# Kernel optimization log

Hardware: AMD Instinct MI355X
Metric: run time of the kernel (lower is better)

## Reference

```python
import jax, jax.numpy as jnp
import numpy as np

N = 100000   # points
C = 256      # in_planes
K = 16       # nsample (idx holds 2*K neighbors)
L = 2        # num_mlplayer
NEG = 0.1    # LeakyReLU slope
EPS = 1e-5   # LayerNorm eps (torch default)

PARAM_KEYS = ['emb_w1','emb_g1','emb_b1','emb_w2','conv_w','pw_w1','pw_g1','pw_b1','pw_w2','pw_g2','pw_b2']


def layer_norm(x, g, b):
    m = x.mean(-1, keepdims=True)
    v = ((x - m) ** 2).mean(-1, keepdims=True)
    return (x - m) * jax.lax.rsqrt(v + EPS) * g + b


def calc_ppf(p, n, pg, ng):
    # standard 4-dim point-pair features: angle(n1,d), angle(n2,d), angle(n1,n2), ||d||
    d = pg - p[:, None, :]                                   # [N,2K,3]
    dist = jnp.linalg.norm(d, axis=-1, keepdims=True)
    def angle(a, b):
        cr = jnp.linalg.norm(jnp.cross(a, b), axis=-1, keepdims=True)
        dt = jnp.sum(a * b, axis=-1, keepdims=True)
        return jnp.arctan2(cr, dt)
    n1 = jnp.broadcast_to(n[:, None, :], pg.shape)
    return jnp.concatenate([angle(n1, d), angle(ng, d), angle(n1, ng), dist], -1)


def mlp_layer(p, x, idx, ppf, r, pr):
    # cart2sphere -> r-normalized radial distance, giving 4+1=5 embedding inputs
    d = p[idx] - p[:, None, :]                               # [N,K,3]
    sphere = jnp.linalg.norm(d, axis=-1, keepdims=True) / r  # [N,K,1]
    f5 = jnp.concatenate([ppf, sphere], -1)                  # [N,K,5]
    h = f5 @ pr['emb_w1']
    h = jax.nn.leaky_relu(layer_norm(h, pr['emb_g1'], pr['emb_b1']), NEG)
    pos = h @ pr['emb_w2']                                   # [N,K,C]
    g = x[idx] + pos                                         # gather + add
    # Partial_conv3 (split_cat): 1x1 conv (no bias) on first C//4 channels
    c4 = pr['conv_w'].shape[0]
    g1 = jnp.einsum('nkc,dc->nkd', g[..., :c4], pr['conv_w'])
    g = jnp.concatenate([g1, g[..., c4:]], -1)
    pooled = g.max(axis=1)                                   # max-pool over neighbors [N,C]
    h = pooled @ pr['pw_w1']
    h = jax.nn.leaky_relu(layer_norm(h, pr['pw_g1'], pr['pw_b1']), NEG)
    h = layer_norm(h @ pr['pw_w2'], pr['pw_g2'], pr['pw_b2'])
    return jax.nn.relu(h + x)                                # residual + relu


def setup_inputs():
    key = jax.random.key(0)
    ks = jax.random.split(key, 16)
    s = 0.02
    n = jax.random.normal(ks[2], (N, 3), jnp.float32)
    n = n / jnp.linalg.norm(n, axis=-1, keepdims=True)
    return {
        'p': jax.random.normal(ks[0], (N, 3), jnp.float32),
        'x': jax.random.normal(ks[1], (N, C), jnp.float32),
        'n': n,
        'idx': jax.random.randint(ks[3], (N, 2 * K), 0, N, jnp.int32),
        'r': jnp.ones((1,), jnp.float32),
        'emb_w1': jax.random.normal(ks[4], (L, 5, C), jnp.float32) * s,
        'emb_g1': jnp.ones((L, C), jnp.float32),
        'emb_b1': jnp.zeros((L, C), jnp.float32),
        'emb_w2': jax.random.normal(ks[5], (L, C, C), jnp.float32) * s,
        'conv_w': jax.random.normal(ks[6], (L, C // 4, C // 4), jnp.float32) * s,
        'pw_w1': jax.random.normal(ks[7], (L, C, 4 * C), jnp.float32) * s,
        'pw_g1': jnp.ones((L, 4 * C), jnp.float32),
        'pw_b1': jnp.zeros((L, 4 * C), jnp.float32),
        'pw_w2': jax.random.normal(ks[8], (L, 4 * C, C), jnp.float32) * s,
        'pw_g2': jnp.ones((L, C), jnp.float32),
        'pw_b2': jnp.zeros((L, C), jnp.float32),
        'proj_w': jax.random.normal(ks[9], (C, C), jnp.float32) * s,
        'proj_b': jnp.zeros((C,), jnp.float32),
    }


def reference(p, x, n, idx, r, emb_w1, emb_g1, emb_b1, emb_w2, conv_w,
              pw_w1, pw_g1, pw_b1, pw_w2, pw_g2, pw_b2, proj_w, proj_b):
    # idx is given -> group_idx = idx (queryandgroup branch skipped, as in source)
    ppf = calc_ppf(p, n, p[idx], n[idx])                     # [N,2K,4]
    idx_m, ppf_m = idx[:, :K], ppf[:, :K]                    # mlp branch uses first nsample
    stacked = [emb_w1, emb_g1, emb_b1, emb_w2, conv_w, pw_w1, pw_g1, pw_b1, pw_w2, pw_g2, pw_b2]
    h = x
    for l in range(L):
        pr = dict(zip(PARAM_KEYS, [a[l] for a in stacked]))
        h = mlp_layer(p, h, idx_m, ppf_m, r[0], pr)
    # proj_mlp; blocks=1 -> trans_block is an empty Sequential (identity)
    return h @ proj_w + proj_b
```

## Files before the change

### kernel.cpp

```cpp
#include <hip/hip_runtime.h>
#include <stdint.h>

#define N_PTS 100000
#define NPAD  100032

typedef unsigned short u16;
typedef unsigned int   u32;
using bf16x8 = __attribute__((ext_vector_type(8))) short;
using f32x4  = __attribute__((ext_vector_type(4))) float;

__device__ __forceinline__ u16 f2bf(float f) {
    u32 u = __float_as_uint(f);
    u += 0x7FFFu + ((u >> 16) & 1u);
    return (u16)(u >> 16);
}
__device__ __forceinline__ float bf2f(u16 h) {
    return __uint_as_float(((u32)h) << 16);
}

__global__ __launch_bounds__(256) void k_transpose_pad(
    const float* __restrict__ src, u16* __restrict__ dst,
    int Lc, int R, int Cc, int stride) {
    int t = blockIdx.x * 256 + threadIdx.x;
    int total = Lc * Cc * stride;
    if (t >= total) return;
    int l = t / (Cc * stride);
    int rem = t - l * (Cc * stride);
    int co = rem / stride;
    int ci = rem - co * stride;
    dst[t] = (ci < R) ? f2bf(src[((size_t)l * R + ci) * Cc + co]) : (u16)0;
}

__global__ __launch_bounds__(256) void k_cast_bf16(
    const float* __restrict__ src, u16* __restrict__ dst, int total) {
    int t = blockIdx.x * 256 + threadIdx.x;
    if (t < total) dst[t] = f2bf(src[t]);
}

__global__ __launch_bounds__(256) void k_castx8(
    const float* __restrict__ src, u16* __restrict__ dst, int total8) {
    int t = blockIdx.x * 256 + threadIdx.x;
    if (t >= total8) return;
    float4 a = *(const float4*)(src + (size_t)t * 8);
    float4 b = *(const float4*)(src + (size_t)t * 8 + 4);
    uint4 o;
    o.x = (u32)f2bf(a.x) | ((u32)f2bf(a.y) << 16);
    o.y = (u32)f2bf(a.z) | ((u32)f2bf(a.w) << 16);
    o.z = (u32)f2bf(b.x) | ((u32)f2bf(b.y) << 16);
    o.w = (u32)f2bf(b.z) | ((u32)f2bf(b.w) << 16);
    *(uint4*)(dst + (size_t)t * 8) = o;
}

__device__ __forceinline__ float angf(float ax, float ay, float az,
                                      float bx, float by, float bz) {
    float cx = ay * bz - az * by;
    float cy = az * bx - ax * bz;
    float cz = ax * by - ay * bx;
    float cr = sqrtf(cx * cx + cy * cy + cz * cz);
    float dt = ax * bx + ay * by + az * bz;
    return atan2f(cr, dt);
}

__global__ __launch_bounds__(256) void k_ppf(
    const float* __restrict__ p, const float* __restrict__ nrm,
    const int* __restrict__ idx, const float* __restrict__ r,
    u16* __restrict__ f5b) {
    int t = blockIdx.x * 256 + threadIdx.x;
    if (t >= N_PTS * 16) return;
    int i = t >> 4;
    int j = idx[(size_t)i * 32 + (t & 15)];
    float pix = p[(size_t)i*3], piy = p[(size_t)i*3+1], piz = p[(size_t)i*3+2];
    float pjx = p[(size_t)j*3], pjy = p[(size_t)j*3+1], pjz = p[(size_t)j*3+2];
    float dx = pjx - pix, dy = pjy - piy, dz = pjz - piz;
    float dist = sqrtf(dx*dx + dy*dy + dz*dz);
    float nix = nrm[(size_t)i*3], niy = nrm[(size_t)i*3+1], niz = nrm[(size_t)i*3+2];
    float njx = nrm[(size_t)j*3], njy = nrm[(size_t)j*3+1], njz = nrm[(size_t)j*3+2];
    float a1 = angf(nix, niy, niz, dx, dy, dz);
    float a2 = angf(njx, njy, njz, dx, dy, dz);
    float a3 = angf(nix, niy, niz, njx, njy, njz);
    float rinv = 1.0f / r[0];
    u16* o = f5b + (size_t)t * 5;
    o[0] = f2bf(a1); o[1] = f2bf(a2); o[2] = f2bf(a3);
    o[3] = f2bf(dist); o[4] = f2bf(dist * rinv);
}

__device__ __forceinline__ bf16x8 fixup_frag(const uint2* pk, int kt,
                                             int srcA, int srcB, bool hiT) {
    int aLx = __shfl((int)pk[2*kt].x,   srcA);
    int aHx = __shfl((int)pk[2*kt+1].x, srcA);
    int aLy = __shfl((int)pk[2*kt].y,   srcA);
    int aHy = __shfl((int)pk[2*kt+1].y, srcA);
    int bLx = __shfl((int)pk[2*kt].x,   srcB);
    int bHx = __shfl((int)pk[2*kt+1].x, srcB);
    int bLy = __shfl((int)pk[2*kt].y,   srcB);
    int bHy = __shfl((int)pk[2*kt+1].y, srcB);
    uint4 u;
    u.x = (u32)(hiT ? aHx : aLx);
    u.y = (u32)(hiT ? aHy : aLy);
    u.z = (u32)(hiT ? bHx : bLx);
    u.w = (u32)(hiT ? bHy : bLy);
    return *(bf16x8*)&u;
}

__global__ __launch_bounds__(512, 4) void k_neighbor(
    const u16*   __restrict__ xcur,
    const u16*   __restrict__ f5b,
    const int*   __restrict__ idx,
    const u16*   __restrict__ w1pad,
    const float* __restrict__ g1, const float* __restrict__ b1,
    const u16*   __restrict__ ew2tp,
    const u16*   __restrict__ convbf,
    u16*         __restrict__ pooledb)
{
    __shared__ u16 Bs[64 * 264];
    __shared__ u16 posw[8][2][16][72];
    __shared__ u16 pbounce[8][2][256];
    __shared__ int idxs[16][16];

    const int tid = threadIdx.x, w = tid >> 6, lane = tid & 63;
    const int rr = lane & 15, q = lane >> 4;
    const int i0 = blockIdx.x * 16;

    for (int o = tid * 16; o < 33792; o += 8192)
        *(uint4*)((char*)Bs + o) = *(const uint4*)((const char*)ew2tp + o);
    if (tid < 256)
        idxs[tid >> 4][tid & 15] = idx[(size_t)(i0 + (tid >> 4)) * 32 + (tid & 15)];

    const int srcA = rr + ((q & 1) << 5);
    const int srcB = srcA + 16;
    const bool hiT = (q >> 1) != 0;

    bf16x8 hfrag[2][8];
    #pragma unroll
    for (int rt = 0; rt < 2; ++rt) {
        const int pt = i0 + 2 * w + rt;
        bf16x8 a1;
        #pragma unroll
        for (int e = 0; e < 8; ++e) a1[e] = 0;
        if (q == 0) {
            const u16* fp = f5b + (size_t)(pt * 16 + rr) * 5;
            a1[0] = (short)fp[0]; a1[1] = (short)fp[1];
            a1[2] = (short)fp[2]; a1[3] = (short)fp[3];
            a1[4] = (short)fp[4];
        }
        f32x4 hacc[16];
        __builtin_amdgcn_s_setprio(1);
        #pragma unroll
        for (int ct = 0; ct < 16; ++ct) {
            bf16x8 aW = *(const bf16x8*)&w1pad[(ct * 16 + rr) * 32 + q * 8];
            f32x4 z = {0.f, 0.f, 0.f, 0.f};
            hacc[ct] = __builtin_amdgcn_mfma_f32_16x16x32_bf16(aW, a1, z, 0, 0, 0);
        }
        __builtin_amdgcn_s_setprio(0);
        float s = 0.f, z2 = 0.f;
        #pragma unroll
        for (int ct = 0; ct < 16; ++ct) {
            #pragma unroll
            for (int j = 0; j < 4; ++j) { float v = hacc[ct][j]; s += v; z2 += v * v; }
        }
        s  += __shfl_xor(s, 16);  s  += __shfl_xor(s, 32);
        z2 += __shfl_xor(z2, 16); z2 += __shfl_xor(z2, 32);
        float mean = s * (1.f / 256.f);
        float var = fmaxf(z2 * (1.f / 256.f) - mean * mean, 0.f);
        float rstd = 1.0f / sqrtf(var + 1e-5f);

        uint2 pk[16];
        #pragma unroll
        for (int ct = 0; ct < 16; ++ct) {
            const int c0 = ct * 16 + 4 * q;
            float4 gg = *(const float4*)&g1[c0];
            float4 bb = *(const float4*)&b1[c0];
            float v0 = (hacc[ct][0] - mean) * rstd * gg.x + bb.x;
            float v1 = (hacc[ct][1] - mean) * rstd * gg.y + bb.y;
            float v2 = (hacc[ct][2] - mean) * rstd * gg.z + bb.z;
            float v3 = (hacc[ct][3] - mean) * rstd * gg.w + bb.w;
            v0 = v0 > 0.f ? v0 : 0.1f * v0;
            v1 = v1 > 0.f ? v1 : 0.1f * v1;
            v2 = v2 > 0.f ? v2 : 0.1f * v2;
            v3 = v3 > 0.f ? v3 : 0.1f * v3;
            pk[ct].x = (u32)f2bf(v0) | ((u32)f2bf(v1) << 16);
            pk[ct].y = (u32)f2bf(v2) | ((u32)f2bf(v3) << 16);
        }
        #pragma unroll
        for (int kt = 0; kt < 8; ++kt)
            hfrag[rt][kt] = fixup_frag(pk, kt, srcA, srcB, hiT);
    }
    __syncthreads();

    const int ppt = lane >> 5, cl = lane & 31;
    const int* ixp = idxs[2 * w + ppt];

    #pragma unroll 1
    for (int p = 0; p < 4; ++p) {
        __builtin_amdgcn_s_setprio(1);
        #pragma unroll
        for (int nt4 = 0; nt4 < 4; ++nt4) {
            f32x4 a0 = {0.f,0.f,0.f,0.f}, a1v = {0.f,0.f,0.f,0.f};
            #pragma unroll
            for (int kb = 0; kb < 8; ++kb) {
                bf16x8 bb = *(const bf16x8*)&Bs[(nt4 * 16 + rr) * 264 + kb * 32 + q * 8];
                a0  = __builtin_amdgcn_mfma_f32_16x16x32_bf16(hfrag[0][kb], bb, a0, 0, 0, 0);
                a1v = __builtin_amdgcn_mfma_f32_16x16x32_bf16(hfrag[1][kb], bb, a1v, 0, 0, 0);
            }
            #pragma unroll
            for (int j = 0; j < 4; ++j) {
                posw[w][0][4 * q + j][nt4 * 16 + rr] = f2bf(a0[j]);
                posw[w][1][4 * q + j][nt4 * 16 + rr] = f2bf(a1v[j]);
            }
        }
        __builtin_amdgcn_s_setprio(0);
        if (p < 3) {
            __syncthreads();
            const char* src = (const char*)(ew2tp + (size_t)(p + 1) * 64 * 264);
            for (int o = tid * 16; o < 33792; o += 8192)
                *(uint4*)((char*)Bs + o) = *(const uint4*)(src + o);
        }
        if (p == 0) {
            #pragma unroll
            for (int pt = 0; pt < 2; ++pt) {
                const u16* xr = xcur + (size_t)idxs[2 * w + pt][rr] * 256;
                bf16x8 gA[2];
                #pragma unroll
                for (int kb = 0; kb < 2; ++kb) {
                    bf16x8 xa = *(const bf16x8*)(xr + kb * 32 + q * 8);
                    bf16x8 pv = *(const bf16x8*)&posw[w][pt][rr][kb * 32 + q * 8];
                    bf16x8 g;
                    #pragma unroll
                    for (int e = 0; e < 8; ++e)
                        g[e] = (short)f2bf(bf2f((u16)xa[e]) + bf2f((u16)pv[e]));
                    gA[kb] = g;
                }
                __builtin_amdgcn_s_setprio(1);
                #pragma unroll
                for (int cn = 0; cn < 4; ++cn) {
                    bf16x8 cB0 = *(const bf16x8*)&convbf[(cn * 16 + rr) * 64 + q * 8];
                    bf16x8 cB1 = *(const bf16x8*)&convbf[(cn * 16 + rr) * 64 + 32 + q * 8];
                    f32x4 z = {0.f,0.f,0.f,0.f};
                    f32x4 acc = __builtin_amdgcn_mfma_f32_16x16x32_bf16(gA[0], cB0, z, 0, 0, 0);
                    acc = __builtin_amdgcn_mfma_f32_16x16x32_bf16(gA[1], cB1, acc, 0, 0, 0);
                    float m = fmaxf(fmaxf(acc[0], acc[1]), fmaxf(acc[2], acc[3]));
                    m = fmaxf(m, __shfl_xor(m, 16));
                    m = fmaxf(m, __shfl_xor(m, 32));
                    if (lane < 16) pbounce[w][pt][cn * 16 + lane] = f2bf(m);
                }
                __builtin_amdgcn_s_setprio(0);
            }
        } else {
            const int cq = p * 64 + cl * 2;
            u32 xv[16];
            #pragma unroll
            for (int k = 0; k < 16; ++k)
                xv[k] = *(const u32*)(xcur + (size_t)ixp[k] * 256 + cq);
            float m0 = -3e38f, m1 = -3e38f;
            #pragma unroll
            for (int k = 0; k < 16; ++k) {
                u32 pv = *(const u32*)&posw[w][ppt][k][cl * 2];
                float gv0 = bf2f((u16)(pv & 0xffffu)) + bf2f((u16)(xv[k] & 0xffffu));
                float gv1 = bf2f((u16)(pv >> 16))     + bf2f((u16)(xv[k] >> 16));
                m0 = fmaxf(m0, gv0);
                m1 = fmaxf(m1, gv1);
            }
            *(u32*)&pbounce[w][ppt][cq] = (u32)f2bf(m0) | ((u32)f2bf(m1) << 16);
        }
        if (p < 3) __syncthreads();
    }
    {
        const int pt = lane >> 5, off = (lane & 31) * 8;
        uint4 v = *(const uint4*)&pbounce[w][pt][off];
        *(uint4*)(pooledb + (size_t)(i0 + 2 * w + pt) * 256 + off) = v;
    }
}

__global__ __launch_bounds__(512, 4) void k_pointwise(
    const u16* poolb,
    const u16* __restrict__ xresb,
    u16*       outb,
    const u16* __restrict__ b1t,
    const float* __restrict__ g1, const float* __restrict__ b1,
    const u16* __restrict__ b2t,
    const float* __restrict__ g2, const float* __restrict__ b2,
    int guardRes)
{
    __shared__ u16 hm[32 * 1032];
    __shared__ float pst[32][8][2];

    const int tid = threadIdx.x, w = tid >> 6, lane = tid & 63;
    const int rr = lane & 15, q = lane >> 4;
    const size_t R0 = (size_t)blockIdx.x * 32;

    bf16x8 afr[2][8];
    #pragma unroll
    for (int rt = 0; rt < 2; ++rt) {
        int ar = (int)R0 + rt * 16 + rr; if (ar >= N_PTS) ar = N_PTS - 1;
        const u16* arow = poolb + (size_t)ar * 256;
        #pragma unroll
        for (int kb = 0; kb < 8; ++kb)
            afr[rt][kb] = *(const bf16x8*)(arow + kb * 32 + q * 8);
    }

    #pragma unroll 2
    for (int ct = 0; ct < 8; ++ct) {
        const int co = w * 128 + ct * 16 + rr;
        const u16* bp = b1t + (size_t)co * 256 + q * 8;
        bf16x8 bb[8];
        #pragma unroll
        for (int kb = 0; kb < 8; ++kb) bb[kb] = *(const bf16x8*)(bp + kb * 32);
        f32x4 a0 = {0.f,0.f,0.f,0.f}, a1v = {0.f,0.f,0.f,0.f};
        __builtin_amdgcn_s_setprio(1);
        #pragma unroll
        for (int kb = 0; kb < 8; ++kb) {
            a0  = __builtin_amdgcn_mfma_f32_16x16x32_bf16(afr[0][kb], bb[kb], a0, 0, 0, 0);
            a1v = __builtin_amdgcn_mfma_f32_16x16x32_bf16(afr[1][kb], bb[kb], a1v, 0, 0, 0);
        }
        __builtin_amdgcn_s_setprio(0);
        #pragma unroll
        for (int j = 0; j < 4; ++j) {
            hm[(4 * q + j) * 1032 + co]      = f2bf(a0[j]);
            hm[(16 + 4 * q + j) * 1032 + co] = f2bf(a1v[j]);
        }
    }
    __syncthreads();

    {
        const int row = tid >> 4;
        const int t16 = tid & 15;
        u32* hm32 = (u32*)hm;
        const int base = row * 516;
        float s = 0.f, z = 0.f;
        #pragma unroll 8
        for (int e = 0; e < 32; ++e) {
            u32 pk = hm32[base + t16 + 16 * e];
            float v0 = bf2f((u16)(pk & 0xffffu)), v1 = bf2f((u16)(pk >> 16));
            s += v0 + v1; z += v0 * v0 + v1 * v1;
        }
        s += __shfl_xor(s, 1); s += __shfl_xor(s, 2);
        s += __shfl_xor(s, 4); s += __shfl_xor(s, 8);
        z += __shfl_xor(z, 1); z += __shfl_xor(z, 2);
        z += __shfl_xor(z, 4); z += __shfl_xor(z, 8);
        float mean = s * (1.f / 1024.f);
        float var = fmaxf(z * (1.f / 1024.f) - mean * mean, 0.f);
        float rstd = 1.0f / sqrtf(var + 1e-5f);
        #pragma unroll 4
        for (int e = 0; e < 32; ++e) {
            const int cidx = t16 + 16 * e;
            u32 pk = hm32[base + cidx];
            const int c = cidx * 2;
            float2 gg = *(const float2*)&g1[c];
            float2 bbv = *(const float2*)&b1[c];
            float v0 = (bf2f((u16)(pk & 0xffffu)) - mean) * rstd * gg.x + bbv.x;
            float v1 = (bf2f((u16)(pk >> 16))     - mean) * rstd * gg.y + bbv.y;
            v0 = v0 > 0.f ? v0 : 0.1f * v0;
            v1 = v1 > 0.f ? v1 : 0.1f * v1;
            hm32[base + cidx] = (u32)f2bf(v0) | ((u32)f2bf(v1) << 16);
        }
    }
    __syncthreads();

    f32x4 acc2[2][2];
    #pragma unroll
    for (int ct = 0; ct < 2; ++ct) {
        const int cB = w * 32 + ct * 16 + rr;
        const u16* bp = b2t + (size_t)cB * 1024 + q * 8;
        f32x4 c0 = {0.f,0.f,0.f,0.f}, c1 = {0.f,0.f,0.f,0.f};
        __builtin_amdgcn_s_setprio(1);
        #pragma unroll 8
        for (int kb = 0; kb < 32; ++kb) {
            bf16x8 b  = *(const bf16x8*)(bp + kb * 32);
            bf16x8 a0 = *(const bf16x8*)&hm[rr * 1032 + kb * 32 + q * 8];
            bf16x8 a1 = *(const bf16x8*)&hm[(16 + rr) * 1032 + kb * 32 + q * 8];
            c0 = __builtin_amdgcn_mfma_f32_16x16x32_bf16(a0, b, c0, 0, 0, 0);
            c1 = __builtin_amdgcn_mfma_f32_16x16x32_bf16(a1, b, c1, 0, 0, 0);
        }
        __builtin_amdgcn_s_setprio(0);
        acc2[0][ct] = c0; acc2[1][ct] = c1;
    }

    #pragma unroll
    for (int rt = 0; rt < 2; ++rt) {
        #pragma unroll
        for (int j = 0; j < 4; ++j) {
            float s = acc2[rt][0][j] + acc2[rt][1][j];
            float z = acc2[rt][0][j] * acc2[rt][0][j] + acc2[rt][1][j] * acc2[rt][1][j];
            s += __shfl_xor(s, 1); s += __shfl_xor(s, 2);
            s += __shfl_xor(s, 4); s += __shfl_xor(s, 8);
            z += __shfl_xor(z, 1); z += __shfl_xor(z, 2);
            z += __shfl_xor(z, 4); z += __shfl_xor(z, 8);
            if (rr == 0) {
                pst[rt * 16 + 4 * q + j][w][0] = s;
                pst[rt * 16 + 4 * q + j][w][1] = z;
            }
        }
    }
    __syncthreads();

    #pragma unroll
    for (int rt = 0; rt < 2; ++rt) {
        float mean2[4], rstd2[4];
        #pragma unroll
        for (int j = 0; j < 4; ++j) {
            const int row = rt * 16 + 4 * q + j;
            float s = 0.f, z = 0.f;
            #pragma unroll
            for (int k = 0; k < 8; ++k) { s += pst[row][k][0]; z += pst[row][k][1]; }
            float mean = s * (1.f / 256.f);
            float var = fmaxf(z * (1.f / 256.f) - mean * mean, 0.f);
            mean2[j] = mean;
            rstd2[j] = 1.0f / sqrtf(var + 1e-5f);
        }
        #pragma unroll
        for (int ct = 0; ct < 2; ++ct) {
            const int c = w * 32 + ct * 16 + rr;
            const float gg = g2[c], bb = b2[c];
            #pragma unroll
            for (int j = 0; j < 4; ++j) {
                const size_t row = R0 + rt * 16 + 4 * q + j;
                float v = (acc2[rt][ct][j] - mean2[j]) * rstd2[j] * gg + bb;
                float xv = 0.f;
                if (!guardRes || row < (size_t)N_PTS) xv = bf2f(xresb[row * 256 + c]);
                float o = v + xv;
                outb[row * 256 + c] = f2bf(o > 0.f ? o : 0.f);
            }
        }
    }
}

__global__ __launch_bounds__(512, 4) void k_proj(
    const u16*   __restrict__ xinb,
    const u16*   __restrict__ pjtp,
    const float* __restrict__ pb,
    float*       __restrict__ out)
{
    __shared__ u16 Bs[128 * 264];
    const int tid = threadIdx.x, w = tid >> 6, lane = tid & 63;
    const int rr = lane & 15, q = lane >> 4;
    const size_t R0 = (size_t)blockIdx.x * 128 + (size_t)w * 16;

    int arn = (int)R0 + rr; if (arn >= N_PTS) arn = N_PTS - 1;
    const u16* arow = xinb + (size_t)arn * 256;
    bf16x8 afr[8];
    #pragma unroll
    for (int kb = 0; kb < 8; ++kb)
        afr[kb] = *(const bf16x8*)(arow + kb * 32 + q * 8);

    #pragma unroll 1
    for (int h = 0; h < 2; ++h) {
        if (h) __syncthreads();
        for (int o = tid * 16; o < 67584; o += 8192)
            *(uint4*)((char*)Bs + o) = *(const uint4*)((const char*)(pjtp + h * 128 * 264) + o);
        __syncthreads();
        #pragma unroll 2
        for (int nt8 = 0; nt8 < 8; ++nt8) {
            f32x4 acc = {0.f, 0.f, 0.f, 0.f};
            __builtin_amdgcn_s_setprio(1);
            #pragma unroll
            for (int kb = 0; kb < 8; ++kb) {
                bf16x8 b = *(const bf16x8*)&Bs[(nt8 * 16 + rr) * 264 + kb * 32 + q * 8];
                acc = __builtin_amdgcn_mfma_f32_16x16x32_bf16(afr[kb], b, acc, 0, 0, 0);
            }
            __builtin_amdgcn_s_setprio(0);
            const int c = h * 128 + nt8 * 16 + rr;
            const float bias = pb[c];
            #pragma unroll
            for (int j = 0; j < 4; ++j) {
                const size_t row = R0 + 4 * q + j;
                if (row < (size_t)N_PTS) out[row * 256 + c] = acc[j] + bias;
            }
        }
    }
}

extern "C" void kernel_launch(void* const* d_in, const int* in_sizes, int n_in,
                              void* d_out, int out_size, void* d_ws, size_t ws_size,
                              hipStream_t stream) {
    const float* p      = (const float*)d_in[0];
    const float* x      = (const float*)d_in[1];
    const float* nn     = (const float*)d_in[2];
    const int*   idx    = (const int*)d_in[3];
    const float* r      = (const float*)d_in[4];
    const float* emb_w1 = (const float*)d_in[5];
    const float* emb_g1 = (const float*)d_in[6];
    const float* emb_b1 = (const float*)d_in[7];
    const float* emb_w2 = (const float*)d_in[8];
    const float* conv_w = (const float*)d_in[9];
    const float* pw_w1  = (const float*)d_in[10];
    const float* pw_g1  = (const float*)d_in[11];
    const float* pw_b1  = (const float*)d_in[12];
    const float* pw_w2  = (const float*)d_in[13];
    const float* pw_g2  = (const float*)d_in[14];
    const float* pw_b2  = (const float*)d_in[15];
    const float* proj_w = (const float*)d_in[16];
    const float* proj_b = (const float*)d_in[17];
    float* out = (float*)d_out;

    char* ws = (char*)d_ws;
    const size_t SZB = (size_t)NPAD * 256 * sizeof(u16);
    u16* xb0 = (u16*)ws;
    u16* PB  = (u16*)(ws + SZB);
    u16* h1B = (u16*)(ws + 2 * SZB);
    u16* f5b = (u16*)(ws + 3 * SZB);
    u16* wb  = f5b + (size_t)N_PTS * 16 * 5;
    u16* ew2tp  = wb;
    u16* pjtp   = ew2tp + 2 * 256 * 264;
    u16* w1pad  = pjtp + 256 * 264;
    u16* convbf = w1pad + 2 * 256 * 32;
    u16* b1t    = convbf + 2 * 64 * 64;
    u16* b2t    = b1t + 2 * 1024 * 256;

    k_transpose_pad<<<(2*256*264 + 255)/256, 256, 0, stream>>>(emb_w2, ew2tp, 2, 256, 256, 264);
    k_transpose_pad<<<(256*264 + 255)/256, 256, 0, stream>>>(proj_w, pjtp, 1, 256, 256, 264);
    k_transpose_pad<<<(2*256*32 + 255)/256, 256, 0, stream>>>(emb_w1, w1pad, 2, 5, 256, 32);
    k_transpose_pad<<<(2*1024*256 + 255)/256, 256, 0, stream>>>(pw_w1, b1t, 2, 256, 1024, 256);
    k_transpose_pad<<<(2*256*1024 + 255)/256, 256, 0, stream>>>(pw_w2, b2t, 2, 1024, 256, 1024);
    k_cast_bf16<<<(2*64*64 + 255)/256, 256, 0, stream>>>(conv_w, convbf, 2*64*64);

    k_castx8<<<(N_PTS*256/8 + 255)/256, 256, 0, stream>>>(x, xb0, N_PTS*256/8);
    k_ppf<<<(N_PTS * 16 + 255)/256, 256, 0, stream>>>(p, nn, idx, r, f5b);

    k_neighbor<<<N_PTS/16, 512, 0, stream>>>(xb0, f5b, idx, w1pad, emb_g1, emb_b1,
                                             ew2tp, convbf, PB);
    k_pointwise<<<NPAD/32, 512, 0, stream>>>(PB, xb0, h1B, b1t, pw_g1, pw_b1,
                                             b2t, pw_g2, pw_b2, 1);
    k_neighbor<<<N_PTS/16, 512, 0, stream>>>(h1B, f5b, idx, w1pad + 256*32,
                                             emb_g1 + 256, emb_b1 + 256,
                                             ew2tp + 256*264, convbf + 64*64, xb0);
    k_pointwise<<<NPAD/32, 512, 0, stream>>>(xb0, h1B, PB, b1t + 1024*256,
                                             pw_g1 + 1024, pw_b1 + 1024,
                                             b2t + 256*1024, pw_g2 + 256, pw_b2 + 256, 0);
    k_proj<<<(NPAD + 127)/128, 512, 0, stream>>>(PB, pjtp, proj_b, out);
}
```

Baseline: 2.127 ms.

## Halve neighbor-kernel LDS staging to 32-column chunks and double occupancy hint

The neighbor kernel now stages the embedding weight in 32-column chunks instead of 64, which roughly halves its shared-memory buffers. It raises the launch-bounds minimum blocks per CU from 4 to 8. The 4-iteration loop is unrolled into an 8-stage explicit schedule in which gathered x loads for the pooling path are issued a stage ahead and consumed across two pooling stages. This aims for more resident blocks to hide gather latency, at the cost of twice as many barriers and weight-staging rounds and tighter register limits that could cause spills.

```diff
diff --git a/kernel.cpp b/kernel.cpp
--- a/kernel.cpp
+++ b/kernel.cpp
@@ -102,7 +102,7 @@
     return *(bf16x8*)&u;
 }
 
-__global__ __launch_bounds__(512, 4) void k_neighbor(
+__global__ __launch_bounds__(512, 8) void k_neighbor(
     const u16*   __restrict__ xcur,
     const u16*   __restrict__ f5b,
     const int*   __restrict__ idx,
@@ -112,8 +112,8 @@
     const u16*   __restrict__ convbf,
     u16*         __restrict__ pooledb)
 {
-    __shared__ u16 Bs[64 * 264];
-    __shared__ u16 posw[8][2][16][72];
+    __shared__ u16 Bs[32 * 264];
+    __shared__ u16 posw[8][2][16][40];
     __shared__ u16 pbounce[8][2][256];
     __shared__ int idxs[16][16];
 
@@ -121,7 +121,7 @@
     const int rr = lane & 15, q = lane >> 4;
     const int i0 = blockIdx.x * 16;
 
-    for (int o = tid * 16; o < 33792; o += 8192)
+    for (int o = tid * 16; o < 16896; o += 8192)
         *(uint4*)((char*)Bs + o) = *(const uint4*)((const char*)ew2tp + o);
     if (tid < 256)
         idxs[tid >> 4][tid & 15] = idx[(size_t)(i0 + (tid >> 4)) * 32 + (tid & 15)];
@@ -190,80 +190,139 @@
     const int ppt = lane >> 5, cl = lane & 31;
     const int* ixp = idxs[2 * w + ppt];
 
-    #pragma unroll 1
-    for (int p = 0; p < 4; ++p) {
+    auto do_gemm = [&]() {
         __builtin_amdgcn_s_setprio(1);
         #pragma unroll
-        for (int nt4 = 0; nt4 < 4; ++nt4) {
+        for (int nt2 = 0; nt2 < 2; ++nt2) {
             f32x4 a0 = {0.f,0.f,0.f,0.f}, a1v = {0.f,0.f,0.f,0.f};
             #pragma unroll
             for (int kb = 0; kb < 8; ++kb) {
-                bf16x8 bb = *(const bf16x8*)&Bs[(nt4 * 16 + rr) * 264 + kb * 32 + q * 8];
+                bf16x8 bb = *(const bf16x8*)&Bs[(nt2 * 16 + rr) * 264 + kb * 32 + q * 8];
                 a0  = __builtin_amdgcn_mfma_f32_16x16x32_bf16(hfrag[0][kb], bb, a0, 0, 0, 0);
                 a1v = __builtin_amdgcn_mfma_f32_16x16x32_bf16(hfrag[1][kb], bb, a1v, 0, 0, 0);
             }
             #pragma unroll
             for (int j = 0; j < 4; ++j) {
-                posw[w][0][4 * q + j][nt4 * 16 + rr] = f2bf(a0[j]);
-                posw[w][1][4 * q + j][nt4 * 16 + rr] = f2bf(a1v[j]);
+                posw[w][0][4 * q + j][nt2 * 16 + rr] = f2bf(a0[j]);
+                posw[w][1][4 * q + j][nt2 * 16 + rr] = f2bf(a1v[j]);
             }
         }
         __builtin_amdgcn_s_setprio(0);
-        if (p < 3) {
-            __syncthreads();
-            const char* src = (const char*)(ew2tp + (size_t)(p + 1) * 64 * 264);
-            for (int o = tid * 16; o < 33792; o += 8192)
-                *(uint4*)((char*)Bs + o) = *(const uint4*)(src + o);
-        }
-        if (p == 0) {
-            #pragma unroll
-            for (int pt = 0; pt < 2; ++pt) {
-                const u16* xr = xcur + (size_t)idxs[2 * w + pt][rr] * 256;
-                bf16x8 gA[2];
-                #pragma unroll
-                for (int kb = 0; kb < 2; ++kb) {
-                    bf16x8 xa = *(const bf16x8*)(xr + kb * 32 + q * 8);
-                    bf16x8 pv = *(const bf16x8*)&posw[w][pt][rr][kb * 32 + q * 8];
-                    bf16x8 g;
-                    #pragma unroll
-                    for (int e = 0; e < 8; ++e)
-                        g[e] = (short)f2bf(bf2f((u16)xa[e]) + bf2f((u16)pv[e]));
-                    gA[kb] = g;
-                }
-                __builtin_amdgcn_s_setprio(1);
-                #pragma unroll
-                for (int cn = 0; cn < 4; ++cn) {
-                    bf16x8 cB0 = *(const bf16x8*)&convbf[(cn * 16 + rr) * 64 + q * 8];
-                    bf16x8 cB1 = *(const bf16x8*)&convbf[(cn * 16 + rr) * 64 + 32 + q * 8];
-                    f32x4 z = {0.f,0.f,0.f,0.f};
-                    f32x4 acc = __builtin_amdgcn_mfma_f32_16x16x32_bf16(gA[0], cB0, z, 0, 0, 0);
-                    acc = __builtin_amdgcn_mfma_f32_16x16x32_bf16(gA[1], cB1, acc, 0, 0, 0);
-                    float m = fmaxf(fmaxf(acc[0], acc[1]), fmaxf(acc[2], acc[3]));
-                    m = fmaxf(m, __shfl_xor(m, 16));
-                    m = fmaxf(m, __shfl_xor(m, 32));
-                    if (lane < 16) pbounce[w][pt][cn * 16 + lane] = f2bf(m);
-                }
-                __builtin_amdgcn_s_setprio(0);
-            }
-        } else {
-            const int cq = p * 64 + cl * 2;
-            u32 xv[16];
-            #pragma unroll
-            for (int k = 0; k < 16; ++k)
-                xv[k] = *(const u32*)(xcur + (size_t)ixp[k] * 256 + cq);
+    };
+    auto stage_e = [&](int en) {
+        const char* src = (const char*)(ew2tp + (size_t)en * 32 * 264);
+        for (int o = tid * 16; o < 16896; o += 8192)
+            *(uint4*)((char*)Bs + o) = *(const uint4*)(src + o);
+    };
+    auto load_pair = [&](int pi, u32 (&xv)[16]) {
+        const int cq = pi * 64 + cl * 2;
+        #pragma unroll
+        for (int k = 0; k < 16; ++k)
+            xv[k] = *(const u32*)(xcur + (size_t)ixp[k] * 256 + cq);
+    };
+    auto pool_e = [&](int e, const u32 (&xv)[16]) {
+        if ((cl >> 4) == (e & 1)) {
+            const int t2 = (cl & 15) * 2;
             float m0 = -3e38f, m1 = -3e38f;
             #pragma unroll
             for (int k = 0; k < 16; ++k) {
-                u32 pv = *(const u32*)&posw[w][ppt][k][cl * 2];
-                float gv0 = bf2f((u16)(pv & 0xffffu)) + bf2f((u16)(xv[k] & 0xffffu));
-                float gv1 = bf2f((u16)(pv >> 16))     + bf2f((u16)(xv[k] >> 16));
-                m0 = fmaxf(m0, gv0);
-                m1 = fmaxf(m1, gv1);
-            }
-            *(u32*)&pbounce[w][ppt][cq] = (u32)f2bf(m0) | ((u32)f2bf(m1) << 16);
-        }
-        if (p < 3) __syncthreads();
-    }
+                u32 pv = *(const u32*)&posw[w][ppt][k][t2];
+                m0 = fmaxf(m0, bf2f((u16)(pv & 0xffffu)) + bf2f((u16)(xv[k] & 0xffffu)));
+                m1 = fmaxf(m1, bf2f((u16)(pv >> 16))     + bf2f((u16)(xv[k] >> 16)));
+            }
+            *(u32*)&pbounce[w][ppt][(e >> 1) * 64 + cl * 2] =
+                (u32)f2bf(m0) | ((u32)f2bf(m1) << 16);
+        }
+    };
+
+    bf16x8 gA0[2], gA1[2];
+    u32 xv[16];
+
+    do_gemm();
+    __syncthreads();
+    stage_e(1);
+    #pragma unroll
+    for (int pt = 0; pt < 2; ++pt) {
+        const u16* xr = xcur + (size_t)idxs[2 * w + pt][rr] * 256;
+        bf16x8 xa = *(const bf16x8*)(xr + q * 8);
+        bf16x8 pv = *(const bf16x8*)&posw[w][pt][rr][q * 8];
+        bf16x8 g;
+        #pragma unroll
+        for (int e = 0; e < 8; ++e)
+            g[e] = (short)f2bf(bf2f((u16)xa[e]) + bf2f((u16)pv[e]));
+        gA0[pt] = g;
+    }
+    __syncthreads();
+
+    do_gemm();
+    __syncthreads();
+    stage_e(2);
+    #pragma unroll
+    for (int pt = 0; pt < 2; ++pt) {
+        const u16* xr = xcur + (size_t)idxs[2 * w + pt][rr] * 256;
+        bf16x8 xa = *(const bf16x8*)(xr + 32 + q * 8);
+        bf16x8 pv = *(const bf16x8*)&posw[w][pt][rr][q * 8];
+        bf16x8 g;
+        #pragma unroll
+        for (int e = 0; e < 8; ++e)
+            g[e] = (short)f2bf(bf2f((u16)xa[e]) + bf2f((u16)pv[e]));
+        gA1[pt] = g;
+    }
+    #pragma unroll
+    for (int pt = 0; pt < 2; ++pt) {
+        __builtin_amdgcn_s_setprio(1);
+        #pragma unroll
+        for (int cn = 0; cn < 4; ++cn) {
+            bf16x8 cB0 = *(const bf16x8*)&convbf[(cn * 16 + rr) * 64 + q * 8];
+            bf16x8 cB1 = *(const bf16x8*)&convbf[(cn * 16 + rr) * 64 + 32 + q * 8];
+            f32x4 z = {0.f,0.f,0.f,0.f};
+            f32x4 acc = __builtin_amdgcn_mfma_f32_16x16x32_bf16(gA0[pt], cB0, z, 0, 0, 0);
+            acc = __builtin_amdgcn_mfma_f32_16x16x32_bf16(gA1[pt], cB1, acc, 0, 0, 0);
+            float m = fmaxf(fmaxf(acc[0], acc[1]), fmaxf(acc[2], acc[3]));
+            m = fmaxf(m, __shfl_xor(m, 16));
+            m = fmaxf(m, __shfl_xor(m, 32));
+            if (lane < 16) pbounce[w][pt][cn * 16 + lane] = f2bf(m);
+        }
+        __builtin_amdgcn_s_setprio(0);
+    }
+    load_pair(1, xv);
+    __syncthreads();
+
+    do_gemm();
+    __syncthreads();
+    stage_e(3);
+    pool_e(2, xv);
+    __syncthreads();
+
+    do_gemm();
+    __syncthreads();
+    stage_e(4);
+    pool_e(3, xv);
+    load_pair(2, xv);
+    __syncthreads();
+
+    do_gemm();
+    __syncthreads();
+    stage_e(5);
+    pool_e(4, xv);
+    __syncthreads();
+
+    do_gemm();
+    __syncthreads();
+    stage_e(6);
+    pool_e(5, xv);
+    load_pair(3, xv);
+    __syncthreads();
+
+    do_gemm();
+    __syncthreads();
+    stage_e(7);
+    pool_e(6, xv);
+    __syncthreads();
+
+    do_gemm();
+    pool_e(7, xv);
+
     {
         const int pt = lane >> 5, off = (lane & 31) * 8;
         uint4 v = *(const uint4*)&pbounce[w][pt][off];
```

New measurement: 2.537 ms. +19.2%, slower.
